# Kernel optimization log

Measured on AMD Instinct MI355X. Metric: run time of the kernel, lower is better.

Reference implementation:

```python
import jax, jax.numpy as jnp
import numpy as np

NEG_SLOPE = 0.2  # LeakyReLU negative slope (act_negative)


def setup_inputs() -> dict:
    key = jax.random.key(0)
    ks = jax.random.split(key, 5)
    B, N, D = 64, 4096, 16
    x = jax.random.normal(ks[0], (B, N, D), dtype=jnp.float32)
    # random adjacency, scaled so row sums are O(1) and activations stay stable
    adj = jax.random.uniform(ks[1], (N, N), dtype=jnp.float32) * (2.0 / N)
    Identity = jnp.eye(N, dtype=jnp.float32)
    W0 = jax.random.normal(ks[2], (D, D), dtype=jnp.float32) * (1.0 / np.sqrt(D))
    W1 = jax.random.normal(ks[3], (D, D), dtype=jnp.float32) * (1.0 / np.sqrt(D))
    W2 = jax.random.normal(ks[4], (D, D), dtype=jnp.float32) * (1.0 / np.sqrt(D))
    return {"x": x, "adj": adj, "Identity": Identity, "W0": W0, "W1": W1, "W2": W2}


def _gcn_layer(x, W, adj, I):
    # GCNConv: linear (no bias) -> leaky_relu -> batched adjacency matmul.
    # The same conv (same W) is applied with adj and with Identity, then summed.
    h = jax.nn.leaky_relu(jnp.einsum('bnd,de->bne', x, W), NEG_SLOPE)
    out_adj = jnp.einsum('nm,bmh->bnh', adj, h)  # replaces per-sample torch.mm loop
    out_id = jnp.einsum('nm,bmh->bnh', I, h)
    return out_adj + out_id


def reference(x, adj, Identity, W0, W1, W2):
    out = _gcn_layer(x, W0, adj, Identity)
    out = _gcn_layer(out, W1, adj, Identity)
    out = _gcn_layer(out, W2, adj, Identity)
    return out  # is_residual=False: no shortcut branch
```

## Files before the change

### kernel.cpp

```cpp
#include <hip/hip_runtime.h>
#include <stdint.h>


typedef float  f32x4  __attribute__((ext_vector_type(4)));
typedef unsigned short ushort8 __attribute__((ext_vector_type(8)));
typedef int    i32x4  __attribute__((ext_vector_type(4)));
typedef int    i32x8  __attribute__((ext_vector_type(8)));

typedef __attribute__((address_space(1))) void* as1p;
typedef __attribute__((address_space(3))) void* as3p;
#define GLOAD_LDS16(G, L) \
  __builtin_amdgcn_global_load_lds((as1p)(G), (as3p)(L), 16, 0, 0)

#define ADJ_SCALE 4096.0f
#define ADJ_DESCALE (1.0f / 4096.0f)
#define SCALE_ONE 0x7f7f7f7f

__device__ __forceinline__ unsigned short f2bf(float f) {
  unsigned u = __float_as_uint(f);
  u += 0x7fffu + ((u >> 16) & 1u);
  return (unsigned short)(u >> 16);
}
__device__ __forceinline__ float bf2f(unsigned short u) {
  return __uint_as_float(((unsigned)u) << 16);
}
__device__ __forceinline__ int pk4_fp8(float a, float b, float c, float d) {
  int v = __builtin_amdgcn_cvt_pk_fp8_f32(a, b, 0, false);
  v = __builtin_amdgcn_cvt_pk_fp8_f32(c, d, v, true);
  return v;
}

__global__ void prep(const float* __restrict__ adj,
                     unsigned char* __restrict__ a8,
                     const float* __restrict__ x,
                     const float* __restrict__ W,
                     unsigned char* __restrict__ hb8,
                     unsigned short* __restrict__ hnc_out) {
  __shared__ float xs[64 * 65];
  __shared__ unsigned short ht[64 * 72];
  int bid = blockIdx.x;

  if (bid >= 1024) {
    size_t base = ((size_t)(bid - 1024) * 256 + threadIdx.x) * 16;
    const float4* src = (const float4*)(adj + base);
    float4 q0 = src[0], q1 = src[1], q2 = src[2], q3 = src[3];
    int4 o;
    o.x = pk4_fp8(q0.x * ADJ_SCALE, q0.y * ADJ_SCALE, q0.z * ADJ_SCALE, q0.w * ADJ_SCALE);
    o.y = pk4_fp8(q1.x * ADJ_SCALE, q1.y * ADJ_SCALE, q1.z * ADJ_SCALE, q1.w * ADJ_SCALE);
    o.z = pk4_fp8(q2.x * ADJ_SCALE, q2.y * ADJ_SCALE, q2.z * ADJ_SCALE, q2.w * ADJ_SCALE);
    o.w = pk4_fp8(q3.x * ADJ_SCALE, q3.y * ADJ_SCALE, q3.z * ADJ_SCALE, q3.w * ADJ_SCALE);
    *(int4*)(a8 + base) = o;
    return;
  }

  int n0 = (bid & 63) * 64, c0 = (bid >> 6) * 64;

  for (int i = threadIdx.x; i < 1024; i += 256) {
    int bs = i >> 8, rem = i & 255, nr = rem >> 2, d4 = rem & 3;
    float4 v = *(const float4*)(
        x + ((size_t)(c0 / 16 + bs) * 4096 + n0 + nr) * 16 + d4 * 4);
    float* dst = xs + nr * 65 + bs * 16 + d4 * 4;
    dst[0] = v.x; dst[1] = v.y; dst[2] = v.z; dst[3] = v.w;
  }
  __syncthreads();

  int n_l = threadIdx.x & 63, b_l = threadIdx.x >> 6;
  float xv[16];
#pragma unroll
  for (int d = 0; d < 16; ++d) xv[d] = xs[n_l * 65 + b_l * 16 + d];
  float accv[16];
#pragma unroll
  for (int e = 0; e < 16; ++e) accv[e] = 0.f;
#pragma unroll
  for (int d = 0; d < 16; ++d)
#pragma unroll
    for (int e = 0; e < 16; ++e) accv[e] += xv[d] * W[d * 16 + e];

  ushort8 h0, h1;
#pragma unroll
  for (int e = 0; e < 16; ++e) {
    float a = accv[e] > 0.f ? accv[e] : 0.2f * accv[e];
    unsigned short hv = f2bf(a);
    ht[(b_l * 16 + e) * 72 + n_l] = hv;
    if (e < 8) h0[e] = hv; else h1[e - 8] = hv;
  }
  unsigned short* ho = hnc_out + (size_t)(n0 + n_l) * 1024 + c0 + b_l * 16;
  *(ushort8*)(ho)     = h0;
  *(ushort8*)(ho + 8) = h1;
  __syncthreads();

  for (int i = threadIdx.x; i < 512; i += 256) {
    int row = i >> 3, ch = i & 7;
    const unsigned short* s = ht + row * 72 + ch * 8;
    int2 v;
    v.x = pk4_fp8(bf2f(s[0]), bf2f(s[1]), bf2f(s[2]), bf2f(s[3]));
    v.y = pk4_fp8(bf2f(s[4]), bf2f(s[5]), bf2f(s[6]), bf2f(s[7]));
    *(int2*)(hb8 + (size_t)(c0 + row) * 4096 + n0 + ch * 8) = v;
  }
}

__global__ __launch_bounds__(512, 1)
void gemm_f8(const unsigned char* __restrict__ A,
             const unsigned char* __restrict__ B8,
             const float* __restrict__ Wn,
             unsigned short* __restrict__ hnc,
             unsigned char* __restrict__ hb8o,
             float* __restrict__ out,
             int mode) {
  const int K = 4096;
  __shared__ unsigned char smem[98304];
  unsigned char* a_s[2] = {smem,         smem + 16384};
  unsigned char* b_s[2] = {smem + 32768, smem + 49152};

  int tid = threadIdx.x, wave = tid >> 6, lane = tid & 63;

  int lin = blockIdx.x;
  int xcd = lin & 7, g = lin >> 3;
  int mth = g & 3, ct = g >> 2;
  int mt = mth * 8 + xcd;
  int n0 = mt * 128, c0 = ct * 128;

  int l8 = lane >> 3, lc = lane & 7;
  int swc = lc ^ l8;
  const unsigned char* gA[2];
  const unsigned char* gB[2];
#pragma unroll
  for (int j = 0; j < 2; ++j) {
    int r = wave * 16 + j * 8 + l8;
    gA[j] = A  + (size_t)(n0 + r) * K + swc * 16;
    gB[j] = B8 + (size_t)(c0 + r) * K + swc * 16;
  }

  int i16 = lane & 15, q = lane >> 4;
  int wm = wave >> 2, wn = wave & 3;
  int sw7 = i16 & 7;
  int pc0 = ((2 * q) ^ sw7) * 16;
  int pc1 = ((2 * q + 1) ^ sw7) * 16;

#define STAGE(buf, it)                                                \
  do {                                                                \
    int k0_ = (it) * 128;                                             \
    _Pragma("unroll")                                                 \
    for (int j = 0; j < 2; ++j) {                                     \
      GLOAD_LDS16(gA[j] + k0_, a_s[buf] + (wave * 16 + j * 8) * 128); \
      GLOAD_LDS16(gB[j] + k0_, b_s[buf] + (wave * 16 + j * 8) * 128); \
    }                                                                 \
  } while (0)

#define COMPUTE(buf)                                                  \
  do {                                                                \
    i32x8 bv[2];                                                      \
    _Pragma("unroll")                                                 \
    for (int u = 0; u < 2; ++u) {                                     \
      const unsigned char* bp = b_s[buf] + (wn * 32 + u * 16 + i16) * 128; \
      i32x4 blo = *(const i32x4*)(bp + pc0);                          \
      i32x4 bhi = *(const i32x4*)(bp + pc1);                          \
      bv[u] = __builtin_shufflevector(blo, bhi, 0, 1, 2, 3, 4, 5, 6, 7); \
    }                                                                 \
    __builtin_amdgcn_s_setprio(1);                                    \
    _Pragma("unroll")                                                 \
    for (int t = 0; t < 4; ++t) {                                     \
      const unsigned char* ap = a_s[buf] + (wm * 64 + t * 16 + i16) * 128; \
      i32x4 alo = *(const i32x4*)(ap + pc0);                          \
      i32x4 ahi = *(const i32x4*)(ap + pc1);                          \
      i32x8 av = __builtin_shufflevector(alo, ahi, 0, 1, 2, 3, 4, 5, 6, 7); \
      _Pragma("unroll")                                               \
      for (int u = 0; u < 2; ++u)                                     \
        acc[t][u] = __builtin_amdgcn_mfma_scale_f32_16x16x128_f8f6f4( \
            av, bv[u], acc[t][u], 0, 0, 0, SCALE_ONE, 0, SCALE_ONE);  \
    }                                                                 \
    __builtin_amdgcn_s_setprio(0);                                    \
  } while (0)

#define WAITVM4() asm volatile("s_waitcnt vmcnt(4)" ::: "memory")
#define WAITVM0() asm volatile("s_waitcnt vmcnt(0)" ::: "memory")
#define BARX() do { asm volatile("" ::: "memory");                    \
                    __builtin_amdgcn_s_barrier();                     \
                    asm volatile("" ::: "memory"); } while (0)

  f32x4 acc[4][2] = {};

  STAGE(0, 0);
  STAGE(1, 1);

  for (int itb = 0; itb < 30; itb += 2) {
    WAITVM4(); BARX(); COMPUTE(0); BARX(); STAGE(0, itb + 2);
    WAITVM4(); BARX(); COMPUTE(1); BARX(); STAGE(1, itb + 3);
  }
  WAITVM4(); BARX(); COMPUTE(0);
  WAITVM0(); BARX(); COMPUTE(1);

#undef STAGE
#undef COMPUTE
#undef WAITVM4
#undef WAITVM0
#undef BARX

  __syncthreads();
  float* u_lds = (float*)smem;
  unsigned short* ht = (unsigned short*)(smem + 65536);

#pragma unroll
  for (int t = 0; t < 4; ++t)
#pragma unroll
    for (int u = 0; u < 2; ++u)
#pragma unroll
      for (int i = 0; i < 4; ++i) {
        int n_l = wm * 64 + t * 16 + q * 4 + i;
        int c_l = wn * 32 + u * 16 + i16;
        u_lds[n_l * 128 + (c_l ^ (((n_l >> 2) & 1) << 4))] = acc[t][u][i];
      }
  __syncthreads();

  if (mode == 0) {
    for (int s = 0; s < 2; ++s) {
      int item = s * 512 + tid;
      int n_l = item & 127, gi = item >> 7;
      int pg = gi ^ ((n_l >> 2) & 1);
      const float* up = u_lds + n_l * 128 + pg * 16;
      size_t gb = (size_t)(n0 + n_l) * 1024 + c0 + gi * 16;
      ushort8 hn0 = *(const ushort8*)(hnc + gb);
      ushort8 hn1 = *(const ushort8*)(hnc + gb + 8);
      float ud[16];
#pragma unroll
      for (int d = 0; d < 8; ++d) {
        ud[d]     = up[d]     * ADJ_DESCALE + bf2f(hn0[d]);
        ud[d + 8] = up[d + 8] * ADJ_DESCALE + bf2f(hn1[d]);
      }
      float hv[16];
#pragma unroll
      for (int e = 0; e < 16; ++e) hv[e] = 0.f;
#pragma unroll
      for (int d = 0; d < 16; ++d)
#pragma unroll
        for (int e = 0; e < 16; ++e) hv[e] += ud[d] * Wn[d * 16 + e];
      ushort8 o0, o1;
#pragma unroll
      for (int e = 0; e < 16; ++e) {
        float a = hv[e] > 0.f ? hv[e] : 0.2f * hv[e];
        unsigned short hb = f2bf(a);
        if (e < 8) o0[e] = hb; else o1[e - 8] = hb;
        int cr = gi * 16 + e;
        ht[cr * 128 + (((n_l >> 3) ^ (cr & 15)) << 3) + (n_l & 7)] = hb;
      }
      *(ushort8*)(hnc + gb)     = o0;
      *(ushort8*)(hnc + gb + 8) = o1;
    }
    __syncthreads();
    for (int s = 0; s < 4; ++s) {
      int item = s * 512 + tid;
      int c_l = item >> 4, n8 = item & 15;
      const unsigned short* hp = ht + c_l * 128 + ((n8 ^ (c_l & 15)) << 3);
      int2 v;
      v.x = pk4_fp8(bf2f(hp[0]), bf2f(hp[1]), bf2f(hp[2]), bf2f(hp[3]));
      v.y = pk4_fp8(bf2f(hp[4]), bf2f(hp[5]), bf2f(hp[6]), bf2f(hp[7]));
      *(int2*)(hb8o + (size_t)(c0 + c_l) * 4096 + n0 + n8 * 8) = v;
    }
  } else {
    for (int s = 0; s < 2; ++s) {
      int item = s * 512 + tid;
      int n_l = item & 127, gi = item >> 7;
      int pg = gi ^ ((n_l >> 2) & 1);
      const float* up = u_lds + n_l * 128 + pg * 16;
      size_t gb = (size_t)(n0 + n_l) * 1024 + c0 + gi * 16;
      ushort8 hn0 = *(const ushort8*)(hnc + gb);
      ushort8 hn1 = *(const ushort8*)(hnc + gb + 8);
      float v[16];
#pragma unroll
      for (int d = 0; d < 8; ++d) {
        v[d]     = up[d]     * ADJ_DESCALE + bf2f(hn0[d]);
        v[d + 8] = up[d + 8] * ADJ_DESCALE + bf2f(hn1[d]);
      }
      int bb = (c0 >> 4) + gi;
      float* op = out + (size_t)bb * 65536 + (size_t)(n0 + n_l) * 16;
      *(float4*)(op)      = float4{v[0],  v[1],  v[2],  v[3]};
      *(float4*)(op + 4)  = float4{v[4],  v[5],  v[6],  v[7]};
      *(float4*)(op + 8)  = float4{v[8],  v[9],  v[10], v[11]};
      *(float4*)(op + 12) = float4{v[12], v[13], v[14], v[15]};
    }
  }
}

extern "C" void kernel_launch(void* const* d_in, const int* in_sizes, int n_in,
                              void* d_out, int out_size, void* d_ws, size_t ws_size,
                              hipStream_t stream) {
  const float* x   = (const float*)d_in[0];
  const float* adj = (const float*)d_in[1];
  const float* W0  = (const float*)d_in[3];
  const float* W1  = (const float*)d_in[4];
  const float* W2  = (const float*)d_in[5];
  float* out = (float*)d_out;

  char* ws = (char*)d_ws;
  unsigned char*  adj8  = (unsigned char*)ws;
  unsigned char*  hb8_a = (unsigned char*)(ws + 16777216);
  unsigned char*  hb8_b = (unsigned char*)(ws + 20971520);
  unsigned short* hnc   = (unsigned short*)(ws + 25165824);

  prep<<<5120, 256, 0, stream>>>(adj, adj8, x, W0, hb8_a, hnc);
  gemm_f8<<<256, 512, 0, stream>>>(adj8, hb8_a, W1, hnc, hb8_b, out, 0);
  gemm_f8<<<256, 512, 0, stream>>>(adj8, hb8_b, W2, hnc, hb8_a, out, 0);
  gemm_f8<<<256, 512, 0, stream>>>(adj8, hb8_a, (const float*)nullptr,
                                   hnc, (unsigned char*)nullptr, out, 1);
}
```

Measured before the change: 270.7 us.

## Split GEMM K dimension in two with flag-synchronized bf16 partial reduction

Each adjacency GEMM launch now uses 512 blocks that each cover half of K. The first finisher per output tile writes a bf16 partial to workspace, and the second spins on an atomic flag, then adds the partial and runs the epilogue. LDS is cut to 64KB and launch bounds raised so more blocks can be resident, aiming to fill the CUs better than 256 blocks did. The cost is extra global traffic for the partials, a spin-wait dependency between blocks, and bf16 rounding of the partial sums.

Measured after the change: 590.2 us. 118% more time.

```diff
diff --git a/kernel.cpp b/kernel.cpp
--- a/kernel.cpp
+++ b/kernel.cpp
@@ -99,16 +99,19 @@
   }
 }
 
-__global__ __launch_bounds__(512, 1)
-void gemm_f8(const unsigned char* __restrict__ A,
-             const unsigned char* __restrict__ B8,
-             const float* __restrict__ Wn,
-             unsigned short* __restrict__ hnc,
-             unsigned char* __restrict__ hb8o,
-             float* __restrict__ out,
-             int mode) {
+__global__ __launch_bounds__(512, 4)
+void gemm_fused(const unsigned char* __restrict__ A,
+                const unsigned char* __restrict__ B8,
+                const float* __restrict__ Wn,
+                unsigned short* __restrict__ hnc,
+                unsigned char* __restrict__ hb8o,
+                unsigned short* __restrict__ p,
+                unsigned* __restrict__ flags,
+                float* __restrict__ out,
+                int base, int mode) {
   const int K = 4096;
-  __shared__ unsigned char smem[98304];
+  __shared__ unsigned char smem[65536];
+  __shared__ unsigned who;
   unsigned char* a_s[2] = {smem,         smem + 16384};
   unsigned char* b_s[2] = {smem + 32768, smem + 49152};
 
@@ -116,9 +119,11 @@
 
   int lin = blockIdx.x;
   int xcd = lin & 7, g = lin >> 3;
-  int mth = g & 3, ct = g >> 2;
+  int mth = g & 3, ct = (g >> 2) & 7, ks = g >> 5;
   int mt = mth * 8 + xcd;
   int n0 = mt * 128, c0 = ct * 128;
+  int kbase = ks * 2048;
+  int region = mt * 8 + ct;
 
   int l8 = lane >> 3, lc = lane & 7;
   int swc = lc ^ l8;
@@ -127,8 +132,8 @@
 #pragma unroll
   for (int j = 0; j < 2; ++j) {
     int r = wave * 16 + j * 8 + l8;
-    gA[j] = A  + (size_t)(n0 + r) * K + swc * 16;
-    gB[j] = B8 + (size_t)(c0 + r) * K + swc * 16;
+    gA[j] = A  + (size_t)(n0 + r) * K + kbase + swc * 16;
+    gB[j] = B8 + (size_t)(c0 + r) * K + kbase + swc * 16;
   }
 
   int i16 = lane & 15, q = lane >> 4;
@@ -183,7 +188,7 @@
   STAGE(0, 0);
   STAGE(1, 1);
 
-  for (int itb = 0; itb < 30; itb += 2) {
+  for (int itb = 0; itb < 14; itb += 2) {
     WAITVM4(); BARX(); COMPUTE(0); BARX(); STAGE(0, itb + 2);
     WAITVM4(); BARX(); COMPUTE(1); BARX(); STAGE(1, itb + 3);
   }
@@ -196,9 +201,54 @@
 #undef WAITVM0
 #undef BARX
 
-  __syncthreads();
-  float* u_lds = (float*)smem;
-  unsigned short* ht = (unsigned short*)(smem + 65536);
+  if (tid == 0) who = atomicAdd(&flags[region], 1u);
+  __syncthreads();
+  unsigned w = who;
+
+  if (w == (unsigned)base) {
+#pragma unroll
+    for (int t = 0; t < 4; ++t)
+#pragma unroll
+      for (int u = 0; u < 2; ++u)
+#pragma unroll
+        for (int i = 0; i < 4; ++i) {
+          int n_g = n0 + wm * 64 + t * 16 + q * 4 + i;
+          int c_g = c0 + wn * 32 + u * 16 + i16;
+          p[(size_t)n_g * 1024 + c_g] = f2bf(acc[t][u][i] * ADJ_DESCALE);
+        }
+    __threadfence();
+    __syncthreads();
+    if (tid == 0) atomicAdd(&flags[region], 1u);
+    return;
+  }
+
+  if (tid == 0) {
+    while (__hip_atomic_load(&flags[region], __ATOMIC_ACQUIRE,
+                             __HIP_MEMORY_SCOPE_AGENT) < (unsigned)base + 3u)
+      __builtin_amdgcn_s_sleep(8);
+  }
+  __syncthreads();
+  __threadfence();
+
+  if (mode == 1) {
+#pragma unroll
+    for (int t = 0; t < 4; ++t)
+#pragma unroll
+      for (int u = 0; u < 2; ++u)
+#pragma unroll
+        for (int i = 0; i < 4; ++i) {
+          int n_l = wm * 64 + t * 16 + q * 4 + i;
+          int c_l = wn * 32 + u * 16 + i16;
+          size_t gidx = (size_t)(n0 + n_l) * 1024 + c0 + c_l;
+          float v = acc[t][u][i] * ADJ_DESCALE + bf2f(p[gidx]) + bf2f(hnc[gidx]);
+          int c = c0 + c_l;
+          out[(size_t)(c >> 4) * 65536 + (size_t)(n0 + n_l) * 16 + (c & 15)] = v;
+        }
+    return;
+  }
+
+  unsigned short* u_bf = (unsigned short*)smem;
+  unsigned short* ht   = (unsigned short*)(smem + 32768);
 
 #pragma unroll
   for (int t = 0; t < 4; ++t)
@@ -208,76 +258,50 @@
       for (int i = 0; i < 4; ++i) {
         int n_l = wm * 64 + t * 16 + q * 4 + i;
         int c_l = wn * 32 + u * 16 + i16;
-        u_lds[n_l * 128 + (c_l ^ (((n_l >> 2) & 1) << 4))] = acc[t][u][i];
+        size_t gidx = (size_t)(n0 + n_l) * 1024 + c0 + c_l;
+        float uv = acc[t][u][i] * ADJ_DESCALE + bf2f(p[gidx]) + bf2f(hnc[gidx]);
+        u_bf[n_l * 128 + (c_l ^ (((n_l >> 2) & 1) << 4))] = f2bf(uv);
       }
   __syncthreads();
 
-  if (mode == 0) {
-    for (int s = 0; s < 2; ++s) {
-      int item = s * 512 + tid;
-      int n_l = item & 127, gi = item >> 7;
-      int pg = gi ^ ((n_l >> 2) & 1);
-      const float* up = u_lds + n_l * 128 + pg * 16;
-      size_t gb = (size_t)(n0 + n_l) * 1024 + c0 + gi * 16;
-      ushort8 hn0 = *(const ushort8*)(hnc + gb);
-      ushort8 hn1 = *(const ushort8*)(hnc + gb + 8);
-      float ud[16];
-#pragma unroll
-      for (int d = 0; d < 8; ++d) {
-        ud[d]     = up[d]     * ADJ_DESCALE + bf2f(hn0[d]);
-        ud[d + 8] = up[d + 8] * ADJ_DESCALE + bf2f(hn1[d]);
-      }
-      float hv[16];
-#pragma unroll
-      for (int e = 0; e < 16; ++e) hv[e] = 0.f;
-#pragma unroll
-      for (int d = 0; d < 16; ++d)
-#pragma unroll
-        for (int e = 0; e < 16; ++e) hv[e] += ud[d] * Wn[d * 16 + e];
-      ushort8 o0, o1;
-#pragma unroll
-      for (int e = 0; e < 16; ++e) {
-        float a = hv[e] > 0.f ? hv[e] : 0.2f * hv[e];
-        unsigned short hb = f2bf(a);
-        if (e < 8) o0[e] = hb; else o1[e - 8] = hb;
-        int cr = gi * 16 + e;
-        ht[cr * 128 + (((n_l >> 3) ^ (cr & 15)) << 3) + (n_l & 7)] = hb;
-      }
-      *(ushort8*)(hnc + gb)     = o0;
-      *(ushort8*)(hnc + gb + 8) = o1;
+  for (int s = 0; s < 2; ++s) {
+    int item = s * 512 + tid;
+    int n_l = item & 127, gi = item >> 7;
+    int pg = gi ^ ((n_l >> 2) & 1);
+    const unsigned short* up = u_bf + n_l * 128 + pg * 16;
+    float ud[16];
+#pragma unroll
+    for (int d = 0; d < 16; ++d) ud[d] = bf2f(up[d]);
+    float hv[16];
+#pragma unroll
+    for (int e = 0; e < 16; ++e) hv[e] = 0.f;
+#pragma unroll
+    for (int d = 0; d < 16; ++d)
+#pragma unroll
+      for (int e = 0; e < 16; ++e) hv[e] += ud[d] * Wn[d * 16 + e];
+    ushort8 o0, o1;
+#pragma unroll
+    for (int e = 0; e < 16; ++e) {
+      float a = hv[e] > 0.f ? hv[e] : 0.2f * hv[e];
+      unsigned short hb = f2bf(a);
+      if (e < 8) o0[e] = hb; else o1[e - 8] = hb;
+      int cr = gi * 16 + e;
+      ht[cr * 128 + (((n_l >> 3) ^ (cr & 15)) << 3) + (n_l & 7)] = hb;
     }
-    __syncthreads();
-    for (int s = 0; s < 4; ++s) {
-      int item = s * 512 + tid;
-      int c_l = item >> 4, n8 = item & 15;
-      const unsigned short* hp = ht + c_l * 128 + ((n8 ^ (c_l & 15)) << 3);
-      int2 v;
-      v.x = pk4_fp8(bf2f(hp[0]), bf2f(hp[1]), bf2f(hp[2]), bf2f(hp[3]));
-      v.y = pk4_fp8(bf2f(hp[4]), bf2f(hp[5]), bf2f(hp[6]), bf2f(hp[7]));
-      *(int2*)(hb8o + (size_t)(c0 + c_l) * 4096 + n0 + n8 * 8) = v;
-    }
-  } else {
-    for (int s = 0; s < 2; ++s) {
-      int item = s * 512 + tid;
-      int n_l = item & 127, gi = item >> 7;
-      int pg = gi ^ ((n_l >> 2) & 1);
-      const float* up = u_lds + n_l * 128 + pg * 16;
-      size_t gb = (size_t)(n0 + n_l) * 1024 + c0 + gi * 16;
-      ushort8 hn0 = *(const ushort8*)(hnc + gb);
-      ushort8 hn1 = *(const ushort8*)(hnc + gb + 8);
-      float v[16];
-#pragma unroll
-      for (int d = 0; d < 8; ++d) {
-        v[d]     = up[d]     * ADJ_DESCALE + bf2f(hn0[d]);
-        v[d + 8] = up[d + 8] * ADJ_DESCALE + bf2f(hn1[d]);
-      }
-      int bb = (c0 >> 4) + gi;
-      float* op = out + (size_t)bb * 65536 + (size_t)(n0 + n_l) * 16;
-      *(float4*)(op)      = float4{v[0],  v[1],  v[2],  v[3]};
-      *(float4*)(op + 4)  = float4{v[4],  v[5],  v[6],  v[7]};
-      *(float4*)(op + 8)  = float4{v[8],  v[9],  v[10], v[11]};
-      *(float4*)(op + 12) = float4{v[12], v[13], v[14], v[15]};
-    }
+    size_t gb = (size_t)(n0 + n_l) * 1024 + c0 + gi * 16;
+    *(ushort8*)(hnc + gb)     = o0;
+    *(ushort8*)(hnc + gb + 8) = o1;
+  }
+  __syncthreads();
+
+  for (int s = 0; s < 4; ++s) {
+    int item = s * 512 + tid;
+    int c_l = item >> 4, n8 = item & 15;
+    const unsigned short* hp = ht + c_l * 128 + ((n8 ^ (c_l & 15)) << 3);
+    int2 v;
+    v.x = pk4_fp8(bf2f(hp[0]), bf2f(hp[1]), bf2f(hp[2]), bf2f(hp[3]));
+    v.y = pk4_fp8(bf2f(hp[4]), bf2f(hp[5]), bf2f(hp[6]), bf2f(hp[7]));
+    *(int2*)(hb8o + (size_t)(c0 + c_l) * 4096 + n0 + n8 * 8) = v;
   }
 }
 
@@ -296,10 +320,17 @@
   unsigned char*  hb8_a = (unsigned char*)(ws + 16777216);
   unsigned char*  hb8_b = (unsigned char*)(ws + 20971520);
   unsigned short* hnc   = (unsigned short*)(ws + 25165824);
+  unsigned short* p     = (unsigned short*)(ws + 33554432);
+  unsigned*       flags = (unsigned*)(ws + 41943040);
+
+  (void)hipMemsetAsync(flags, 0, 1024, stream);
 
   prep<<<5120, 256, 0, stream>>>(adj, adj8, x, W0, hb8_a, hnc);
-  gemm_f8<<<256, 512, 0, stream>>>(adj8, hb8_a, W1, hnc, hb8_b, out, 0);
-  gemm_f8<<<256, 512, 0, stream>>>(adj8, hb8_b, W2, hnc, hb8_a, out, 0);
-  gemm_f8<<<256, 512, 0, stream>>>(adj8, hb8_a, (const float*)nullptr,
-                                   hnc, (unsigned char*)nullptr, out, 1);
-}
+  gemm_fused<<<512, 512, 0, stream>>>(adj8, hb8_a, W1, hnc, hb8_b, p, flags,
+                                      out, 0, 0);
+  gemm_fused<<<512, 512, 0, stream>>>(adj8, hb8_b, W2, hnc, hb8_a, p, flags,
+                                      out, 3, 0);
+  gemm_fused<<<512, 512, 0, stream>>>(adj8, hb8_a, (const float*)nullptr, hnc,
+                                      (unsigned char*)nullptr, p, flags,
+                                      out, 6, 1);
+}
```
